# Optimization experiments

Measured on AMD Instinct MI355X. Metric: run time of the kernel, lower is better.

The kernel has to match this reference:

```python
import jax, jax.numpy as jnp
import numpy as np

LN_EPS = 1e-5  # ParlAI LAYER_NORM_EPS
B, S, D, H, E, V = 4, 512, 512, 2048, 8, 32000


def setup_inputs() -> dict:
    key = jax.random.key(0)
    ks = jax.random.split(key, 6)
    x = jax.random.normal(ks[0], (B, S, D), dtype=jnp.float32)
    orig_input = jax.random.randint(ks[1], (B, S), 0, V)          # token ids
    hash_bin_map = jax.random.randint(ks[2], (V,), 0, E, dtype=jnp.int32)
    W1 = jax.random.normal(ks[3], (E, D, H), dtype=jnp.float32) * 0.02
    b1 = jnp.zeros((E, H), dtype=jnp.float32)
    W2 = jax.random.normal(ks[4], (E, H, D), dtype=jnp.float32) * 0.02
    b2 = jnp.zeros((E, D), dtype=jnp.float32)
    gamma = jnp.ones((D,), dtype=jnp.float32)
    beta = jnp.zeros((D,), dtype=jnp.float32)
    return {"x": x, "W1": W1, "b1": b1, "W2": W2, "b2": b2,
            "gamma": gamma, "beta": beta,
            "orig_input": orig_input, "hash_bin_map": hash_bin_map}


def _layernorm(z, gamma, beta):
    mu = jnp.mean(z, axis=-1, keepdims=True)
    var = jnp.var(z, axis=-1, keepdims=True)
    return (z - mu) * jax.lax.rsqrt(var + LN_EPS) * gamma + beta


def reference(x, W1, b1, W2, b2, gamma, beta, orig_input, hash_bin_map):
    # per-token expert assignment via hash of token id
    bins = hash_bin_map[orig_input]                    # [B, S] int
    n_experts = W1.shape[0]
    ffn_out = jnp.zeros_like(x)
    # loop over the small fixed expert set; mask-combine replaces gather/scatter
    for e in range(n_experts):
        h = jax.nn.relu(jnp.einsum('bsd,dh->bsh', x, W1[e]) + b1[e])
        y = jnp.einsum('bsh,hd->bsd', h, W2[e]) + b2[e]
        ffn_out = ffn_out + jnp.where((bins == e)[..., None], y, 0.0)
    # residual + shared LayerNorm (every token belongs to exactly one bin)
    return _layernorm(x + ffn_out, gamma, beta)
```

## Files before the change

### kernel.cpp

```cpp
#include <hip/hip_runtime.h>
#include <hip/hip_bf16.h>
#include <stdint.h>

#define D_DIM 512
#define H_DIM 2048
#define E_NUM 8
#define TM 64
#define CAP 2560
#define MAXRT 6

typedef __attribute__((ext_vector_type(8))) short short8;
typedef __attribute__((ext_vector_type(4))) float floatx4;

union Pack4 { short4 u; __hip_bfloat16 h[4]; };

__device__ inline void async16(const void* g, void* s) {
    __builtin_amdgcn_global_load_lds(
        (const __attribute__((address_space(1))) void*)g,
        (__attribute__((address_space(3))) void*)s, 16, 0, 0);
}

__global__ __launch_bounds__(256) void bin_kernel(
    const int* __restrict__ orig, const int* __restrict__ hmap,
    int* __restrict__ gidx, int* __restrict__ meta, int ntok)
{
    __shared__ int cnt[E_NUM];
    __shared__ int cur[E_NUM];
    int tid = threadIdx.x;
    if (tid < E_NUM) cnt[tid] = 0;
    __syncthreads();
    for (int t = tid; t < ntok; t += 256) {
        int b = hmap[orig[t]];
        atomicAdd(&cnt[b], 1);
    }
    __syncthreads();
    if (tid == 0) {
        int off = 0;
        for (int e = 0; e < E_NUM; e++) {
            int ne = cnt[e];
            int nt = (ne + TM - 1) / TM;
            meta[e] = off;
            meta[8 + e] = ne;
            meta[16 + e] = nt;
            cur[e] = off;
            off += nt * TM;
        }
        meta[24] = off;
    }
    __syncthreads();
    for (int t = tid; t < ntok; t += 256) {
        int b = hmap[orig[t]];
        int p = atomicAdd(&cur[b], 1);
        gidx[p] = t;
    }
}

__global__ __launch_bounds__(128) void gather_kernel(
    const float* __restrict__ x, const int* __restrict__ gidx,
    const int* __restrict__ meta, __hip_bfloat16* __restrict__ Xg)
{
    int g = blockIdx.x;
    int e = -1, local = 0;
#pragma unroll
    for (int i = 0; i < E_NUM; i++) {
        int p = meta[i], nt = meta[16 + i];
        if (g >= p && g < p + nt * TM) { e = i; local = g - p; }
    }
    if (e < 0) return;
    int tid = threadIdx.x;
    __hip_bfloat16* orow = Xg + (size_t)g * D_DIM + tid * 4;
    if (local < meta[8 + e]) {
        int t = gidx[g];
        float4 v = ((const float4*)(x + (size_t)t * D_DIM))[tid];
        orow[0] = __float2bfloat16(v.x);
        orow[1] = __float2bfloat16(v.y);
        orow[2] = __float2bfloat16(v.z);
        orow[3] = __float2bfloat16(v.w);
    } else {
        orow[0] = __float2bfloat16(0.f);
        orow[1] = __float2bfloat16(0.f);
        orow[2] = __float2bfloat16(0.f);
        orow[3] = __float2bfloat16(0.f);
    }
}

template <int WN, int ASTRIDE, int KTOT, int KS, bool RELU>
__global__ __launch_bounds__(256) void moe_gemm_kernel(
    const __hip_bfloat16* __restrict__ A,
    const float* __restrict__ W,
    const float* __restrict__ bias,
    __hip_bfloat16* __restrict__ OutBf,
    float* __restrict__ OutF,
    const int* __restrict__ meta)
{
    constexpr int KLEN = KTOT / KS;
    const int e = blockIdx.z;
    const int n0 = blockIdx.x * 64;
    const int ks = blockIdx.y;
    const int kbase = ks * KLEN;

    int nt = meta[16 + e];
    if (nt > MAXRT) nt = MAXRT;
    const int row0 = meta[e];
    const int rows8 = nt * 64 * 8;

    __shared__ __align__(16) __hip_bfloat16 As[384 * 64];
    __shared__ __align__(16) __hip_bfloat16 Bs[64 * 64];

    const int tid = threadIdx.x;
    const int lane = tid & 63, w = tid >> 6;
    const int quad = lane >> 4, l16 = lane & 15;
    const int wr = w >> 1, wc = w & 1;

    const __hip_bfloat16* Ab = A + (size_t)row0 * ASTRIDE + kbase;
    const int kq = tid >> 4;
    const int nb = tid & 15;
    const float* Wb = W + ((size_t)e * KTOT + kbase) * WN + n0;

    floatx4 acc[MAXRT][2][2] = {};

    float4 br[4];
#pragma unroll
    for (int r = 0; r < 4; r++)
        br[r] = *(const float4*)(Wb + (size_t)(kq * 4 + r) * WN + nb * 4);

    for (int k0 = 0; k0 < KLEN; k0 += 64) {
        __syncthreads();
        for (int c = tid; c < rows8; c += 256) {
            int row = c >> 3;
            int kk = ((c & 7) * 16) ^ ((row & 7) * 16);
            async16(Ab + (size_t)row * ASTRIDE + k0 + (kk >> 1), (char*)As + c * 16);
        }
#pragma unroll
        for (int j = 0; j < 4; j++) {
            int n = nb * 4 + j;
            Pack4 pk;
#pragma unroll
            for (int r = 0; r < 4; r++)
                pk.h[r] = __float2bfloat16(reinterpret_cast<const float*>(&br[r])[j]);
            *(short4*)((char*)Bs + n * 128 + ((kq * 8) ^ (((n >> 2) & 7) * 16))) = pk.u;
        }
        __syncthreads();
        if (k0 + 64 < KLEN) {
#pragma unroll
            for (int r = 0; r < 4; r++)
                br[r] = *(const float4*)(Wb + (size_t)(k0 + 64 + kq * 4 + r) * WN + nb * 4);
        }
#pragma unroll
        for (int kf = 0; kf < 2; kf++) {
            int kb = kf * 64 + quad * 16;
            short8 b[2];
#pragma unroll
            for (int ni = 0; ni < 2; ni++) {
                int n = wc * 32 + ni * 16 + l16;
                b[ni] = *(const short8*)((char*)Bs + n * 128 + (kb ^ (((n >> 2) & 7) * 16)));
            }
#pragma unroll
            for (int rt = 0; rt < MAXRT; rt++) {
                if (rt < nt) {
                    short8 a[2];
#pragma unroll
                    for (int mi = 0; mi < 2; mi++) {
                        int row = rt * 64 + wr * 32 + mi * 16 + l16;
                        a[mi] = *(const short8*)((char*)As + row * 128 + (kb ^ ((row & 7) * 16)));
                    }
#pragma unroll
                    for (int mi = 0; mi < 2; mi++)
#pragma unroll
                        for (int ni = 0; ni < 2; ni++)
                            acc[rt][mi][ni] = __builtin_amdgcn_mfma_f32_16x16x32_bf16(
                                a[mi], b[ni], acc[rt][mi][ni], 0, 0, 0);
                }
            }
        }
    }

#pragma unroll
    for (int rt = 0; rt < MAXRT; rt++) {
        if (rt >= nt) break;
#pragma unroll
        for (int ni = 0; ni < 2; ni++) {
            int col = n0 + wc * 32 + ni * 16 + l16;
            float bv = RELU ? bias[e * WN + col] : 0.f;
#pragma unroll
            for (int mi = 0; mi < 2; mi++) {
#pragma unroll
                for (int r = 0; r < 4; r++) {
                    int grow = row0 + rt * 64 + wr * 32 + mi * 16 + quad * 4 + r;
                    float v = acc[rt][mi][ni][r] + bv;
                    if constexpr (RELU) {
                        v = v > 0.f ? v : 0.f;
                        OutBf[(size_t)grow * WN + col] = __float2bfloat16(v);
                    } else {
                        OutF[((size_t)ks * CAP + grow) * WN + col] = v;
                    }
                }
            }
        }
    }
}

__global__ __launch_bounds__(128) void ln_kernel(
    const float* __restrict__ x, const float* __restrict__ Yb,
    const float* __restrict__ b2,
    const float* __restrict__ gamma, const float* __restrict__ beta,
    const int* __restrict__ gidx, const int* __restrict__ meta,
    float* __restrict__ out)
{
    int g = blockIdx.x;
    int e = -1;
#pragma unroll
    for (int i = 0; i < E_NUM; i++) {
        int p = meta[i], ne = meta[8 + i];
        if (g >= p && g - p < ne) e = i;
    }
    if (e < 0) return;
    int t = gidx[g];
    int tid = threadIdx.x;

    float4 xv = ((const float4*)(x + (size_t)t * D_DIM))[tid];
    float4 bb = ((const float4*)(b2 + (size_t)e * D_DIM))[tid];
    float z0 = xv.x + bb.x, z1 = xv.y + bb.y, z2 = xv.z + bb.z, z3 = xv.w + bb.w;
#pragma unroll
    for (int s4 = 0; s4 < 4; s4++) {
        float4 yv = ((const float4*)(Yb + (size_t)(s4 * CAP + g) * D_DIM))[tid];
        z0 += yv.x; z1 += yv.y; z2 += yv.z; z3 += yv.w;
    }

    float s = z0 + z1 + z2 + z3;
    float ss = z0 * z0 + z1 * z1 + z2 * z2 + z3 * z3;
#pragma unroll
    for (int off = 32; off > 0; off >>= 1) {
        s  += __shfl_down(s, off, 64);
        ss += __shfl_down(ss, off, 64);
    }
    __shared__ float red[4];
    int lane = tid & 63, wv = tid >> 6;
    if (lane == 0) { red[wv] = s; red[2 + wv] = ss; }
    __syncthreads();
    float S = red[0] + red[1];
    float SS = red[2] + red[3];
    float mu = S * (1.f / D_DIM);
    float var = SS * (1.f / D_DIM) - mu * mu;
    float inv = rsqrtf(var + 1e-5f);

    float4 gv = ((const float4*)gamma)[tid];
    float4 bv = ((const float4*)beta)[tid];
    float4 o;
    o.x = (z0 - mu) * inv * gv.x + bv.x;
    o.y = (z1 - mu) * inv * gv.y + bv.y;
    o.z = (z2 - mu) * inv * gv.z + bv.z;
    o.w = (z3 - mu) * inv * gv.w + bv.w;
    ((float4*)(out + (size_t)t * D_DIM))[tid] = o;
}

extern "C" void kernel_launch(void* const* d_in, const int* in_sizes, int n_in,
                              void* d_out, int out_size, void* d_ws, size_t ws_size,
                              hipStream_t stream)
{
    const float* x     = (const float*)d_in[0];
    const float* W1    = (const float*)d_in[1];
    const float* b1    = (const float*)d_in[2];
    const float* W2    = (const float*)d_in[3];
    const float* b2    = (const float*)d_in[4];
    const float* gamma = (const float*)d_in[5];
    const float* beta  = (const float*)d_in[6];
    const int* orig    = (const int*)d_in[7];
    const int* hmap    = (const int*)d_in[8];
    float* out = (float*)d_out;
    int ntok = in_sizes[7];

    char* ws = (char*)d_ws;
    float*          Yb  = (float*)(ws);
    __hip_bfloat16* Hb  = (__hip_bfloat16*)(ws + 20971520);
    __hip_bfloat16* Xg  = (__hip_bfloat16*)(ws + 31457280);
    int*            gidx= (int*)(ws + 34078720);
    int*            meta= (int*)(ws + 34089000 - 10280 + 10240);

    hipLaunchKernelGGL(bin_kernel, dim3(1), dim3(256), 0, stream,
                       orig, hmap, gidx, meta, ntok);
    hipLaunchKernelGGL(gather_kernel, dim3(CAP), dim3(128), 0, stream,
                       x, gidx, meta, Xg);
    hipLaunchKernelGGL((moe_gemm_kernel<H_DIM, D_DIM, D_DIM, 1, true>),
                       dim3(H_DIM / 64, 1, E_NUM), dim3(256), 0, stream,
                       Xg, W1, b1, Hb, (float*)nullptr, meta);
    hipLaunchKernelGGL((moe_gemm_kernel<D_DIM, H_DIM, H_DIM, 4, false>),
                       dim3(D_DIM / 64, 4, E_NUM), dim3(256), 0, stream,
                       Hb, W2, (const float*)nullptr, (__hip_bfloat16*)nullptr, Yb, meta);
    hipLaunchKernelGGL(ln_kernel, dim3(CAP), dim3(128), 0, stream,
                       x, Yb, b2, gamma, beta, gidx, meta, out);
}
```

Baseline: 155.4 us.

## Double-buffer MoE GEMM LDS tiles, stage ReLU output, atomically reduce split-K

Rewrites the expert GEMM main loop to double-buffer both the async-loaded activation tiles (now 32-wide K steps) and the bf16-converted weight tiles, so global loads overlap MFMA work with one barrier per step. The first GEMM's ReLU output is staged through LDS so stores to global memory are coalesced 16-byte writes. The split-K second GEMM now accumulates with float atomics into a single zeroed buffer, zeroed in the gather kernel, so the LayerNorm kernel reads one partial instead of four. The costs are 64KB of LDS per block, which may lower occupancy, atomic contention, and a summation order that is no longer deterministic.

```diff
diff --git a/kernel.cpp b/kernel.cpp
--- a/kernel.cpp
+++ b/kernel.cpp
@@ -39,9 +39,7 @@
         for (int e = 0; e < E_NUM; e++) {
             int ne = cnt[e];
             int nt = (ne + TM - 1) / TM;
-            meta[e] = off;
-            meta[8 + e] = ne;
-            meta[16 + e] = nt;
+            meta[e] = off; meta[8 + e] = ne; meta[16 + e] = nt;
             cur[e] = off;
             off += nt * TM;
         }
@@ -57,9 +55,14 @@
 
 __global__ __launch_bounds__(128) void gather_kernel(
     const float* __restrict__ x, const int* __restrict__ gidx,
-    const int* __restrict__ meta, __hip_bfloat16* __restrict__ Xg)
+    const int* __restrict__ meta, __hip_bfloat16* __restrict__ Xg,
+    float* __restrict__ Yb)
 {
     int g = blockIdx.x;
+    int tid = threadIdx.x;
+    float4 z4 = {0.f, 0.f, 0.f, 0.f};
+    ((float4*)(Yb + (size_t)g * D_DIM))[tid] = z4;
+
     int e = -1, local = 0;
 #pragma unroll
     for (int i = 0; i < E_NUM; i++) {
@@ -67,7 +70,6 @@
         if (g >= p && g < p + nt * TM) { e = i; local = g - p; }
     }
     if (e < 0) return;
-    int tid = threadIdx.x;
     __hip_bfloat16* orow = Xg + (size_t)g * D_DIM + tid * 4;
     if (local < meta[8 + e]) {
         int t = gidx[g];
@@ -94,110 +96,165 @@
     const int* __restrict__ meta)
 {
     constexpr int KLEN = KTOT / KS;
+    constexpr int NI = KLEN / 32;
+    constexpr int NB = KLEN / 64;
     const int e = blockIdx.z;
+    const int ks = blockIdx.y;
     const int n0 = blockIdx.x * 64;
-    const int ks = blockIdx.y;
     const int kbase = ks * KLEN;
 
     int nt = meta[16 + e];
     if (nt > MAXRT) nt = MAXRT;
     const int row0 = meta[e];
-    const int rows8 = nt * 64 * 8;
-
-    __shared__ __align__(16) __hip_bfloat16 As[384 * 64];
-    __shared__ __align__(16) __hip_bfloat16 Bs[64 * 64];
+
+    __shared__ __align__(16) char lds[65536];
+    char* AsB[2] = { lds, lds + 24576 };
+    char* BsB[2] = { lds + 49152, lds + 57344 };
 
     const int tid = threadIdx.x;
     const int lane = tid & 63, w = tid >> 6;
     const int quad = lane >> 4, l16 = lane & 15;
     const int wr = w >> 1, wc = w & 1;
-
-    const __hip_bfloat16* Ab = A + (size_t)row0 * ASTRIDE + kbase;
     const int kq = tid >> 4;
     const int nb = tid & 15;
+
+    const __hip_bfloat16* Ab = A + (size_t)row0 * ASTRIDE + kbase;
     const float* Wb = W + ((size_t)e * KTOT + kbase) * WN + n0;
 
     floatx4 acc[MAXRT][2][2] = {};
-
-    float4 br[4];
-#pragma unroll
-    for (int r = 0; r < 4; r++)
-        br[r] = *(const float4*)(Wb + (size_t)(kq * 4 + r) * WN + nb * 4);
-
-    for (int k0 = 0; k0 < KLEN; k0 += 64) {
+    float4 br_a[4], br_b[4];
+
+#define LOADB(j, br) do {                                                     \
+    _Pragma("unroll")                                                         \
+    for (int r = 0; r < 4; r++)                                               \
+        br[r] = *(const float4*)(Wb + (size_t)((j) * 64 + kq * 4 + r) * WN + nb * 4); \
+} while (0)
+
+#define WRITEB(br, buf) do {                                                  \
+    char* bs = BsB[buf];                                                      \
+    _Pragma("unroll")                                                         \
+    for (int j = 0; j < 4; j++) {                                             \
+        int n = nb * 4 + j;                                                   \
+        Pack4 pk;                                                             \
+        _Pragma("unroll")                                                     \
+        for (int r = 0; r < 4; r++)                                           \
+            pk.h[r] = __float2bfloat16(reinterpret_cast<const float*>(&br[r])[j]); \
+        *(short4*)(bs + n * 128 + ((kq * 8) ^ (((n >> 2) & 7) * 16))) = pk.u; \
+    }                                                                         \
+} while (0)
+
+#define DMA_A(i, buf) do {                                                    \
+    int k0 = (i) * 32;                                                        \
+    char* dst = AsB[buf];                                                     \
+    for (int c = tid; c < nt * 256; c += 256) {                               \
+        int row = c >> 2;                                                     \
+        int ch = (c & 3) ^ ((row + (row >> 2)) & 3);                          \
+        async16(Ab + (size_t)row * ASTRIDE + k0 + ch * 8, dst + c * 16);      \
+    }                                                                         \
+} while (0)
+
+#define COMPUTE(Acur, B2cur, kf) do {                                         \
+    const char* as = AsB[Acur];                                               \
+    const char* bs = BsB[B2cur];                                              \
+    short8 bfr[2];                                                            \
+    _Pragma("unroll")                                                         \
+    for (int ni = 0; ni < 2; ni++) {                                          \
+        int n = wc * 32 + ni * 16 + l16;                                      \
+        bfr[ni] = *(const short8*)(bs + n * 128 +                             \
+                   (((kf) * 64 + quad * 16) ^ (((n >> 2) & 7) * 16)));        \
+    }                                                                         \
+    _Pragma("unroll")                                                         \
+    for (int rt = 0; rt < MAXRT; rt++) {                                      \
+        if (rt < nt) {                                                        \
+            short8 afr[2];                                                    \
+            _Pragma("unroll")                                                 \
+            for (int mi = 0; mi < 2; mi++) {                                  \
+                int row = rt * 64 + wr * 32 + mi * 16 + l16;                  \
+                afr[mi] = *(const short8*)(as + row * 64 +                    \
+                           ((quad ^ ((row + (row >> 2)) & 3)) * 16));         \
+            }                                                                 \
+            _Pragma("unroll")                                                 \
+            for (int mi = 0; mi < 2; mi++)                                    \
+                _Pragma("unroll")                                             \
+                for (int ni = 0; ni < 2; ni++)                                \
+                    acc[rt][mi][ni] = __builtin_amdgcn_mfma_f32_16x16x32_bf16(\
+                        afr[mi], bfr[ni], acc[rt][mi][ni], 0, 0, 0);          \
+        }                                                                     \
+    }                                                                         \
+} while (0)
+
+#define STEP(i, Acur, B2cur, DOB, brW, brL) do {                              \
+    __syncthreads();                                                          \
+    if ((i) + 1 < NI) DMA_A((i) + 1, (Acur) ^ 1);                             \
+    if (DOB) {                                                                \
+        if ((i) / 2 + 1 < NB) WRITEB(brW, (B2cur) ^ 1);                       \
+        if ((i) / 2 + 2 < NB) LOADB((i) / 2 + 2, brL);                        \
+    }                                                                         \
+    COMPUTE(Acur, B2cur, (i) & 1);                                            \
+} while (0)
+
+    LOADB(0, br_a);
+    WRITEB(br_a, 0);
+    LOADB(1, br_a);
+    DMA_A(0, 0);
+
+    for (int i = 0; i < NI; i += 4) {
+        STEP(i + 0, 0, 0, 1, br_a, br_b);
+        STEP(i + 1, 1, 0, 0, br_a, br_b);
+        STEP(i + 2, 0, 1, 1, br_b, br_a);
+        STEP(i + 3, 1, 1, 0, br_a, br_b);
+    }
+
+    if constexpr (RELU) {
         __syncthreads();
-        for (int c = tid; c < rows8; c += 256) {
-            int row = c >> 3;
-            int kk = ((c & 7) * 16) ^ ((row & 7) * 16);
-            async16(Ab + (size_t)row * ASTRIDE + k0 + (kk >> 1), (char*)As + c * 16);
-        }
-#pragma unroll
-        for (int j = 0; j < 4; j++) {
-            int n = nb * 4 + j;
-            Pack4 pk;
-#pragma unroll
-            for (int r = 0; r < 4; r++)
-                pk.h[r] = __float2bfloat16(reinterpret_cast<const float*>(&br[r])[j]);
-            *(short4*)((char*)Bs + n * 128 + ((kq * 8) ^ (((n >> 2) & 7) * 16))) = pk.u;
-        }
-        __syncthreads();
-        if (k0 + 64 < KLEN) {
-#pragma unroll
-            for (int r = 0; r < 4; r++)
-                br[r] = *(const float4*)(Wb + (size_t)(k0 + 64 + kq * 4 + r) * WN + nb * 4);
-        }
-#pragma unroll
-        for (int kf = 0; kf < 2; kf++) {
-            int kb = kf * 64 + quad * 16;
-            short8 b[2];
+#pragma unroll
+        for (int rt = 0; rt < MAXRT; rt++) {
+            if (rt >= nt) break;
 #pragma unroll
             for (int ni = 0; ni < 2; ni++) {
-                int n = wc * 32 + ni * 16 + l16;
-                b[ni] = *(const short8*)((char*)Bs + n * 128 + (kb ^ (((n >> 2) & 7) * 16)));
-            }
-#pragma unroll
-            for (int rt = 0; rt < MAXRT; rt++) {
-                if (rt < nt) {
-                    short8 a[2];
-#pragma unroll
-                    for (int mi = 0; mi < 2; mi++) {
-                        int row = rt * 64 + wr * 32 + mi * 16 + l16;
-                        a[mi] = *(const short8*)((char*)As + row * 128 + (kb ^ ((row & 7) * 16)));
-                    }
-#pragma unroll
-                    for (int mi = 0; mi < 2; mi++)
-#pragma unroll
-                        for (int ni = 0; ni < 2; ni++)
-                            acc[rt][mi][ni] = __builtin_amdgcn_mfma_f32_16x16x32_bf16(
-                                a[mi], b[ni], acc[rt][mi][ni], 0, 0, 0);
-                }
-            }
-        }
-    }
-
-#pragma unroll
-    for (int rt = 0; rt < MAXRT; rt++) {
-        if (rt >= nt) break;
-#pragma unroll
-        for (int ni = 0; ni < 2; ni++) {
-            int col = n0 + wc * 32 + ni * 16 + l16;
-            float bv = RELU ? bias[e * WN + col] : 0.f;
-#pragma unroll
-            for (int mi = 0; mi < 2; mi++) {
-#pragma unroll
-                for (int r = 0; r < 4; r++) {
-                    int grow = row0 + rt * 64 + wr * 32 + mi * 16 + quad * 4 + r;
-                    float v = acc[rt][mi][ni][r] + bv;
-                    if constexpr (RELU) {
+                int col = wc * 32 + ni * 16 + l16;
+                float bv = bias[e * WN + n0 + col];
+#pragma unroll
+                for (int mi = 0; mi < 2; mi++) {
+#pragma unroll
+                    for (int r = 0; r < 4; r++) {
+                        int row = rt * 64 + wr * 32 + mi * 16 + quad * 4 + r;
+                        float v = acc[rt][mi][ni][r] + bv;
                         v = v > 0.f ? v : 0.f;
-                        OutBf[(size_t)grow * WN + col] = __float2bfloat16(v);
-                    } else {
-                        OutF[((size_t)ks * CAP + grow) * WN + col] = v;
+                        *(__hip_bfloat16*)(lds + row * 144 + col * 2) = __float2bfloat16(v);
                     }
                 }
             }
         }
-    }
+        __syncthreads();
+        int totc = nt * 64 * 8;
+        for (int c = tid; c < totc; c += 256) {
+            int row = c >> 3;
+            short8 v = *(const short8*)(lds + row * 144 + (c & 7) * 16);
+            *(short8*)(OutBf + (size_t)(row0 + row) * WN + n0 + (c & 7) * 8) = v;
+        }
+    } else {
+#pragma unroll
+        for (int rt = 0; rt < MAXRT; rt++) {
+            if (rt >= nt) break;
+#pragma unroll
+            for (int mi = 0; mi < 2; mi++)
+#pragma unroll
+                for (int ni = 0; ni < 2; ni++) {
+                    int col = n0 + wc * 32 + ni * 16 + l16;
+#pragma unroll
+                    for (int r = 0; r < 4; r++) {
+                        int grow = row0 + rt * 64 + wr * 32 + mi * 16 + quad * 4 + r;
+                        atomicAdd(&OutF[(size_t)grow * WN + col], acc[rt][mi][ni][r]);
+                    }
+                }
+        }
+    }
+#undef LOADB
+#undef WRITEB
+#undef DMA_A
+#undef COMPUTE
+#undef STEP
 }
 
 __global__ __launch_bounds__(128) void ln_kernel(
@@ -219,13 +276,12 @@
     int tid = threadIdx.x;
 
     float4 xv = ((const float4*)(x + (size_t)t * D_DIM))[tid];
+    float4 yv = ((const float4*)(Yb + (size_t)g * D_DIM))[tid];
     float4 bb = ((const float4*)(b2 + (size_t)e * D_DIM))[tid];
-    float z0 = xv.x + bb.x, z1 = xv.y + bb.y, z2 = xv.z + bb.z, z3 = xv.w + bb.w;
-#pragma unroll
-    for (int s4 = 0; s4 < 4; s4++) {
-        float4 yv = ((const float4*)(Yb + (size_t)(s4 * CAP + g) * D_DIM))[tid];
-        z0 += yv.x; z1 += yv.y; z2 += yv.z; z3 += yv.w;
-    }
+    float z0 = xv.x + yv.x + bb.x;
+    float z1 = xv.y + yv.y + bb.y;
+    float z2 = xv.z + yv.z + bb.z;
+    float z3 = xv.w + yv.w + bb.w;
 
     float s = z0 + z1 + z2 + z3;
     float ss = z0 * z0 + z1 * z1 + z2 * z2 + z3 * z3;
@@ -272,15 +328,15 @@
 
     char* ws = (char*)d_ws;
     float*          Yb  = (float*)(ws);
-    __hip_bfloat16* Hb  = (__hip_bfloat16*)(ws + 20971520);
-    __hip_bfloat16* Xg  = (__hip_bfloat16*)(ws + 31457280);
-    int*            gidx= (int*)(ws + 34078720);
-    int*            meta= (int*)(ws + 34089000 - 10280 + 10240);
+    __hip_bfloat16* Hb  = (__hip_bfloat16*)(ws + 5242880);
+    __hip_bfloat16* Xg  = (__hip_bfloat16*)(ws + 15728640);
+    int*            gidx= (int*)(ws + 18350080);
+    int*            meta= (int*)(ws + 18360320);
 
     hipLaunchKernelGGL(bin_kernel, dim3(1), dim3(256), 0, stream,
                        orig, hmap, gidx, meta, ntok);
     hipLaunchKernelGGL(gather_kernel, dim3(CAP), dim3(128), 0, stream,
-                       x, gidx, meta, Xg);
+                       x, gidx, meta, Xg, Yb);
     hipLaunchKernelGGL((moe_gemm_kernel<H_DIM, D_DIM, D_DIM, 1, true>),
                        dim3(H_DIM / 64, 1, E_NUM), dim3(256), 0, stream,
                        Xg, W1, b1, Hb, (float*)nullptr, meta);
```

Result: slower. 165.0 us (+6.2%).
